# Kernel optimization log

Hardware: AMD Instinct MI355X
Metric: run time of the kernel (lower is better)

The kernel has to match this reference:

```python
import jax, jax.numpy as jnp
import numpy as np

WEIGHT = 0.1
TEMPERATURE = 0.07
EPS_NORM = 1e-12   # F.normalize eps
EPS_DEN = 1e-6     # denominator eps in pos_mask.sum()


def setup_inputs() -> dict:
    key = jax.random.key(0)
    k1, k2 = jax.random.split(key)
    features = jax.random.normal(k1, (4, 1000, 2048), dtype=jnp.float32)
    target = jax.random.randint(k2, (4, 1000), 0, 16, dtype=jnp.int64)
    return {"features": features, "target": target}


def _per_sample_loss(f, t):
    # f: [N, C], t: [N]
    N = f.shape[0]
    # F.normalize(dim=1)
    norm = jnp.maximum(jnp.linalg.norm(f, axis=1, keepdims=True), EPS_NORM)
    f = f / norm
    # [N, N] cosine similarities scaled by temperature
    sim = jnp.matmul(f, f.T) / TEMPERATURE
    eye = jnp.eye(N, dtype=f.dtype)
    pos = (t[:, None] == t[None, :]).astype(f.dtype) * (1.0 - eye)
    neg = 1.0 - pos - eye
    pos_sim = sim * pos
    # -log(exp(pos_sim) / (exp(pos_sim) + sum_j exp(sim)*neg))  summed over ALL entries
    denom = jnp.exp(pos_sim) + jnp.sum(jnp.exp(sim) * neg, axis=1, keepdims=True)
    loss_mat = jnp.log(denom) - pos_sim
    pos_sum = pos.sum()
    return loss_mat.sum() / (pos_sum + EPS_DEN), pos_sum


def reference(features, target):
    # features: [B, N, C] (already 3-D: no subsampling / interpolation paths fire)
    losses, pos_sums = jax.vmap(_per_sample_loss)(features, target)
    valid = pos_sums > 0
    num_pairs = valid.sum().astype(features.dtype)
    total = jnp.where(valid, losses, 0.0).sum()
    return jnp.where(num_pairs > 0, WEIGHT * total / num_pairs,
                     jnp.asarray(WEIGHT * 0.1, dtype=features.dtype))
```

## Files before the change

kernel.cpp:

```cpp
#include <hip/hip_runtime.h>
#include <math.h>

#define BB 4
#define NN 1000
#define NP 1024
#define CC 2048
#define TINV (1.0f / 0.07f)
#define BK 64

#define FNORM_BYTES ((size_t)BB * NP * CC * 2)
#define SIMB_BYTES  ((size_t)2 * BB * NP * NP * 2)
#define RL_BYTES    ((size_t)BB * NP * 4)

typedef __bf16 bf16x8 __attribute__((ext_vector_type(8)));
typedef float  f32x4  __attribute__((ext_vector_type(4)));
typedef float  f32x16 __attribute__((ext_vector_type(16)));

__device__ __forceinline__ void load_lds16(const void* g, void* l) {
    __builtin_amdgcn_global_load_lds(
        (const __attribute__((address_space(1))) unsigned int*)g,
        (__attribute__((address_space(3))) unsigned int*)l, 16, 0, 0);
}

__device__ __forceinline__ float blk_sum(float v, volatile float* lds) {
    int lane = threadIdx.x & 63;
    int wid  = threadIdx.x >> 6;
#pragma unroll
    for (int off = 32; off; off >>= 1) v += __shfl_down(v, off);
    __syncthreads();
    if (lane == 0) lds[wid] = v;
    __syncthreads();
    return lds[0] + lds[1] + lds[2] + lds[3];
}

__device__ __forceinline__ float wave_sum(float v) {
#pragma unroll
    for (int off = 32; off; off >>= 1) v += __shfl_down(v, off);
    return __shfl(v, 0);
}

__global__ __launch_bounds__(256) void norm_bf16_kernel(const float* __restrict__ f,
                                                        __bf16* __restrict__ out) {
    __shared__ float lds[4];
    __shared__ float scale_s;
    const int blk = blockIdx.x;
    const int b = blk >> 10, r = blk & (NP - 1);
    __bf16* dst = out + ((size_t)b * NP + r) * CC;
    const int tid = threadIdx.x;

    if (r >= NN) {
        ((uint4*)dst)[tid] = make_uint4(0u, 0u, 0u, 0u);
        return;
    }
    const float* src = f + ((size_t)b * NN + r) * CC;

    float ss = 0.f;
#pragma unroll
    for (int h = 0; h < 2; ++h) {
        float4 v = ((const float4*)src)[tid + h * 256];
        ss += v.x * v.x + v.y * v.y + v.z * v.z + v.w * v.w;
    }
    float tot = blk_sum(ss, lds);
    if (tid == 0) scale_s = 1.0f / fmaxf(sqrtf(tot), 1e-12f);
    __syncthreads();
    const float sc = scale_s;

    float4 v0 = ((const float4*)src)[tid * 2];
    float4 v1 = ((const float4*)src)[tid * 2 + 1];
    bf16x8 o;
    o[0] = (__bf16)(v0.x * sc); o[1] = (__bf16)(v0.y * sc);
    o[2] = (__bf16)(v0.z * sc); o[3] = (__bf16)(v0.w * sc);
    o[4] = (__bf16)(v1.x * sc); o[5] = (__bf16)(v1.y * sc);
    o[6] = (__bf16)(v1.z * sc); o[7] = (__bf16)(v1.w * sc);
    *(bf16x8*)(dst + tid * 8) = o;
}

__global__ __launch_bounds__(256) void simgemm_mfma(const __bf16* __restrict__ fn,
                                                    __bf16* __restrict__ simb) {
    __shared__ __bf16 As0[128 * BK], As1[128 * BK];
    __shared__ __bf16 Bs0[128 * BK], Bs1[128 * BK];

    const int bz = blockIdx.z;
    const int b  = bz >> 1;
    const int kbeg = (bz & 1) * (CC / 2);
    const int tI = blockIdx.y * 128;
    const int tJ = blockIdx.x * 128;
    const __bf16* base = fn + (size_t)b * NP * CC;
    __bf16* S = simb + (size_t)bz * NP * NP;

    const int tid  = threadIdx.x;
    const int wid  = tid >> 6;
    const int lane = tid & 63;
    const int wm   = wid >> 1;
    const int wn   = wid & 1;
    const int ln32 = lane & 31;
    const int kh   = lane >> 5;
    const int sw   = ln32 & 7;

    const int srow   = tid >> 3;
    const int schunk = (tid & 7) ^ (srow & 7);
    const __bf16* gA = base + (size_t)(tI + srow) * CC + kbeg + schunk * 8;
    const __bf16* gB = base + (size_t)(tJ + srow) * CC + kbeg + schunk * 8;
    const int wvoff = wid * 8 * BK;

    f32x16 acc[2][2] = {};

#define STAGE(k0, A, B)                                                      \
    {                                                                        \
        _Pragma("unroll")                                                    \
        for (int r = 0; r < 4; ++r)                                          \
            load_lds16(gA + (k0) + (size_t)r * 32 * CC, (A) + r * 32 * BK + wvoff); \
        _Pragma("unroll")                                                    \
        for (int r = 0; r < 4; ++r)                                          \
            load_lds16(gB + (k0) + (size_t)r * 32 * CC, (B) + r * 32 * BK + wvoff); \
    }

#define COMPUTE(A, B)                                                        \
    {                                                                        \
        _Pragma("unroll")                                                    \
        for (int kc = 0; kc < 4; ++kc) {                                     \
            const int co = ((kc * 2 + kh) ^ sw) * 8;                         \
            bf16x8 a0 = *(const bf16x8*)&(A)[(wm * 64      + ln32) * BK + co]; \
            bf16x8 a1 = *(const bf16x8*)&(A)[(wm * 64 + 32 + ln32) * BK + co]; \
            bf16x8 b0 = *(const bf16x8*)&(B)[(wn * 64      + ln32) * BK + co]; \
            bf16x8 b1 = *(const bf16x8*)&(B)[(wn * 64 + 32 + ln32) * BK + co]; \
            acc[0][0] = __builtin_amdgcn_mfma_f32_32x32x16_bf16(a0, b0, acc[0][0], 0, 0, 0); \
            acc[0][1] = __builtin_amdgcn_mfma_f32_32x32x16_bf16(a0, b1, acc[0][1], 0, 0, 0); \
            acc[1][0] = __builtin_amdgcn_mfma_f32_32x32x16_bf16(a1, b0, acc[1][0], 0, 0, 0); \
            acc[1][1] = __builtin_amdgcn_mfma_f32_32x32x16_bf16(a1, b1, acc[1][1], 0, 0, 0); \
        }                                                                    \
    }

    STAGE(0, As0, Bs0);
#pragma unroll 1
    for (int k0 = 0; k0 < CC / 2; k0 += 2 * BK) {
        __syncthreads();
        if (k0 + BK < CC / 2) STAGE(k0 + BK, As1, Bs1);
        COMPUTE(As0, Bs0);
        __syncthreads();
        if (k0 + 2 * BK < CC / 2) STAGE(k0 + 2 * BK, As0, Bs0);
        COMPUTE(As1, Bs1);
    }
#undef STAGE
#undef COMPUTE

#pragma unroll
    for (int at = 0; at < 2; ++at) {
#pragma unroll
        for (int bt = 0; bt < 2; ++bt) {
            const int col = tJ + wn * 64 + bt * 32 + ln32;
#pragma unroll
            for (int r = 0; r < 16; ++r) {
                const int row = tI + wm * 64 + at * 32 + (r & 3) + 8 * (r >> 2) + 4 * kh;
                S[(size_t)row * NP + col] = (__bf16)(acc[at][bt][r] * TINV);
            }
        }
    }
}

__global__ __launch_bounds__(256) void rowloss_kernel(const __bf16* __restrict__ simb,
                                                      const int* __restrict__ tgt,
                                                      float* __restrict__ rloss,
                                                      float* __restrict__ rpos) {
    __shared__ __align__(16) int ts[NN];
    __shared__ float rowv[4][NP];
    const int b = blockIdx.y;
    const int wid = threadIdx.x >> 6, lane = threadIdx.x & 63;
    const int* t = tgt + (size_t)b * NN;
    for (int j = threadIdx.x; j < NN; j += 256) ts[j] = t[j];
    __syncthreads();

    const int i = blockIdx.x * 4 + wid;
    const __bf16* r0 = simb + (size_t)(2 * b) * NP * NP + (size_t)i * NP;
    const __bf16* r1 = r0 + (size_t)NP * NP;
    const int ti = ts[i];

    float sneg = 0.f, pcnt = 0.f;
    for (int g = lane; g < NN / 8; g += 64) {
        bf16x8 va = ((const bf16x8*)r0)[g];
        bf16x8 vb = ((const bf16x8*)r1)[g];
        float v[8];
#pragma unroll
        for (int k = 0; k < 8; ++k) v[k] = (float)va[k] + (float)vb[k];
        *(f32x4*)&rowv[wid][g * 8]     = *(f32x4*)&v[0];
        *(f32x4*)&rowv[wid][g * 8 + 4] = *(f32x4*)&v[4];
        const int jb = g * 8;
#pragma unroll
        for (int k = 0; k < 8; ++k) {
            const int j = jb + k;
            if (j != i) {
                if (ts[j] == ti) pcnt += 1.f;
                else             sneg += __expf(v[k]);
            }
        }
    }
    const float Sv = wave_sum(sneg);
    const float p  = wave_sum(pcnt);

    float term = 0.f;
    for (int g = lane; g < NN / 8; g += 64) {
        const int jb = g * 8;
        float v[8];
        *(f32x4*)&v[0] = *(const f32x4*)&rowv[wid][jb];
        *(f32x4*)&v[4] = *(const f32x4*)&rowv[wid][jb + 4];
#pragma unroll
        for (int k = 0; k < 8; ++k) {
            const int j = jb + k;
            if (j != i && ts[j] == ti)
                term += __logf(__expf(v[k]) + Sv) - v[k];
        }
    }
    const float tt = wave_sum(term);
    if (lane == 0) {
        rloss[b * NP + i] = tt + ((float)NN - p) * __logf(1.f + Sv);
        rpos [b * NP + i] = p;
    }
}

__global__ __launch_bounds__(256) void final_kernel(const float* __restrict__ rloss,
                                                    const float* __restrict__ rpos,
                                                    float* __restrict__ out) {
    __shared__ float lds[4];
    float total = 0.f, np = 0.f;
    for (int b = 0; b < BB; ++b) {
        float l = 0.f, p = 0.f;
        for (int i = threadIdx.x; i < NN; i += 256) {
            l += rloss[b * NP + i];
            p += rpos [b * NP + i];
        }
        float ls = blk_sum(l, lds);
        float ps = blk_sum(p, lds);
        if (ps > 0.f) { total += ls / (ps + 1e-6f); np += 1.f; }
    }
    if (threadIdx.x == 0)
        out[0] = (np > 0.f) ? 0.1f * total / np : 0.1f * 0.1f;
}

extern "C" void kernel_launch(void* const* d_in, const int* in_sizes, int n_in,
                              void* d_out, int out_size, void* d_ws, size_t ws_size,
                              hipStream_t stream) {
    const float* feat = (const float*)d_in[0];
    const int*   tgt  = (const int*)d_in[1];
    char* ws = (char*)d_ws;
    __bf16* fnorm = (__bf16*)ws;                  ws += FNORM_BYTES;
    __bf16* simb  = (__bf16*)ws;                  ws += SIMB_BYTES;
    float*  rloss = (float*)ws;                   ws += RL_BYTES;
    float*  rpos  = (float*)ws;

    norm_bf16_kernel<<<dim3(BB * NP), 256, 0, stream>>>(feat, fnorm);
    simgemm_mfma<<<dim3(NP / 128, NP / 128, 2 * BB), 256, 0, stream>>>(fnorm, simb);
    rowloss_kernel<<<dim3(NN / 4, BB), 256, 0, stream>>>(simb, tgt, rloss, rpos);
    final_kernel<<<1, 256, 0, stream>>>(rloss, rpos, (float*)d_out);
}
```

Baseline: 116.1 us.

## Split GEMM K dimension four ways with smaller K tile and higher occupancy

Raises the split-K factor for the similarity GEMM from 2 to 4, which doubles the grid to 1024 blocks. It halves the K tile to 32 with a matching LDS swizzle and staging layout, and adds a launch-bounds occupancy hint of 4 blocks per CU. The goal is to fill the 256 CUs better than 512 blocks did. In exchange, the bf16 partial-sum buffer doubles, and the rowloss kernel must read and add four partial matrices, which increases memory traffic and rounding error.

```diff
diff --git a/kernel.cpp b/kernel.cpp
--- a/kernel.cpp
+++ b/kernel.cpp
@@ -6,10 +6,10 @@
 #define NP 1024
 #define CC 2048
 #define TINV (1.0f / 0.07f)
-#define BK 64
+#define BK 32
 
 #define FNORM_BYTES ((size_t)BB * NP * CC * 2)
-#define SIMB_BYTES  ((size_t)2 * BB * NP * NP * 2)
+#define SIMB_BYTES  ((size_t)4 * BB * NP * NP * 2)
 #define RL_BYTES    ((size_t)BB * NP * 4)
 
 typedef __bf16 bf16x8 __attribute__((ext_vector_type(8)));
@@ -75,14 +75,14 @@
     *(bf16x8*)(dst + tid * 8) = o;
 }
 
-__global__ __launch_bounds__(256) void simgemm_mfma(const __bf16* __restrict__ fn,
-                                                    __bf16* __restrict__ simb) {
+__global__ __launch_bounds__(256, 4) void simgemm_mfma(const __bf16* __restrict__ fn,
+                                                       __bf16* __restrict__ simb) {
     __shared__ __bf16 As0[128 * BK], As1[128 * BK];
     __shared__ __bf16 Bs0[128 * BK], Bs1[128 * BK];
 
     const int bz = blockIdx.z;
-    const int b  = bz >> 1;
-    const int kbeg = (bz & 1) * (CC / 2);
+    const int b  = bz >> 2;
+    const int kbeg = (bz & 3) * (CC / 4);
     const int tI = blockIdx.y * 128;
     const int tJ = blockIdx.x * 128;
     const __bf16* base = fn + (size_t)b * NP * CC;
@@ -95,50 +95,48 @@
     const int wn   = wid & 1;
     const int ln32 = lane & 31;
     const int kh   = lane >> 5;
-    const int sw   = ln32 & 7;
-
-    const int srow   = tid >> 3;
-    const int schunk = (tid & 7) ^ (srow & 7);
+    const int sw   = (ln32 >> 1) & 3;
+
+    const int srow   = wid * 16 + (lane >> 2);
+    const int schunk = (lane & 3) ^ ((srow >> 1) & 3);
     const __bf16* gA = base + (size_t)(tI + srow) * CC + kbeg + schunk * 8;
     const __bf16* gB = base + (size_t)(tJ + srow) * CC + kbeg + schunk * 8;
-    const int wvoff = wid * 8 * BK;
+    const int wvoff = wid * 512;
 
     f32x16 acc[2][2] = {};
 
-#define STAGE(k0, A, B)                                                      \
-    {                                                                        \
-        _Pragma("unroll")                                                    \
-        for (int r = 0; r < 4; ++r)                                          \
-            load_lds16(gA + (k0) + (size_t)r * 32 * CC, (A) + r * 32 * BK + wvoff); \
-        _Pragma("unroll")                                                    \
-        for (int r = 0; r < 4; ++r)                                          \
-            load_lds16(gB + (k0) + (size_t)r * 32 * CC, (B) + r * 32 * BK + wvoff); \
-    }
-
-#define COMPUTE(A, B)                                                        \
-    {                                                                        \
-        _Pragma("unroll")                                                    \
-        for (int kc = 0; kc < 4; ++kc) {                                     \
-            const int co = ((kc * 2 + kh) ^ sw) * 8;                         \
-            bf16x8 a0 = *(const bf16x8*)&(A)[(wm * 64      + ln32) * BK + co]; \
-            bf16x8 a1 = *(const bf16x8*)&(A)[(wm * 64 + 32 + ln32) * BK + co]; \
-            bf16x8 b0 = *(const bf16x8*)&(B)[(wn * 64      + ln32) * BK + co]; \
-            bf16x8 b1 = *(const bf16x8*)&(B)[(wn * 64 + 32 + ln32) * BK + co]; \
+#define STAGE(k0, A, B)                                            \
+    {                                                              \
+        load_lds16(gA + (k0),                   (A) + wvoff);      \
+        load_lds16(gA + (k0) + (size_t)64 * CC, (A) + 2048 + wvoff); \
+        load_lds16(gB + (k0),                   (B) + wvoff);      \
+        load_lds16(gB + (k0) + (size_t)64 * CC, (B) + 2048 + wvoff); \
+    }
+
+#define COMPUTE(A, B)                                                         \
+    {                                                                         \
+        _Pragma("unroll")                                                     \
+        for (int kc = 0; kc < 2; ++kc) {                                      \
+            const int co = ((kc * 2 + kh) ^ sw) * 8;                          \
+            bf16x8 a0 = *(const bf16x8*)&(A)[(wm * 64      + ln32) * BK + co];\
+            bf16x8 a1 = *(const bf16x8*)&(A)[(wm * 64 + 32 + ln32) * BK + co];\
+            bf16x8 b0 = *(const bf16x8*)&(B)[(wn * 64      + ln32) * BK + co];\
+            bf16x8 b1 = *(const bf16x8*)&(B)[(wn * 64 + 32 + ln32) * BK + co];\
             acc[0][0] = __builtin_amdgcn_mfma_f32_32x32x16_bf16(a0, b0, acc[0][0], 0, 0, 0); \
             acc[0][1] = __builtin_amdgcn_mfma_f32_32x32x16_bf16(a0, b1, acc[0][1], 0, 0, 0); \
             acc[1][0] = __builtin_amdgcn_mfma_f32_32x32x16_bf16(a1, b0, acc[1][0], 0, 0, 0); \
             acc[1][1] = __builtin_amdgcn_mfma_f32_32x32x16_bf16(a1, b1, acc[1][1], 0, 0, 0); \
-        }                                                                    \
+        }                                                                     \
     }
 
     STAGE(0, As0, Bs0);
 #pragma unroll 1
-    for (int k0 = 0; k0 < CC / 2; k0 += 2 * BK) {
+    for (int k0 = 0; k0 < CC / 4; k0 += 2 * BK) {
         __syncthreads();
-        if (k0 + BK < CC / 2) STAGE(k0 + BK, As1, Bs1);
+        if (k0 + BK < CC / 4) STAGE(k0 + BK, As1, Bs1);
         COMPUTE(As0, Bs0);
         __syncthreads();
-        if (k0 + 2 * BK < CC / 2) STAGE(k0 + 2 * BK, As0, Bs0);
+        if (k0 + 2 * BK < CC / 4) STAGE(k0 + 2 * BK, As0, Bs0);
         COMPUTE(As1, Bs1);
     }
 #undef STAGE
@@ -171,17 +169,22 @@
     __syncthreads();
 
     const int i = blockIdx.x * 4 + wid;
-    const __bf16* r0 = simb + (size_t)(2 * b) * NP * NP + (size_t)i * NP;
+    const __bf16* r0 = simb + (size_t)(4 * b) * NP * NP + (size_t)i * NP;
     const __bf16* r1 = r0 + (size_t)NP * NP;
+    const __bf16* r2 = r1 + (size_t)NP * NP;
+    const __bf16* r3 = r2 + (size_t)NP * NP;
     const int ti = ts[i];
 
     float sneg = 0.f, pcnt = 0.f;
     for (int g = lane; g < NN / 8; g += 64) {
         bf16x8 va = ((const bf16x8*)r0)[g];
         bf16x8 vb = ((const bf16x8*)r1)[g];
+        bf16x8 vc = ((const bf16x8*)r2)[g];
+        bf16x8 vd = ((const bf16x8*)r3)[g];
         float v[8];
 #pragma unroll
-        for (int k = 0; k < 8; ++k) v[k] = (float)va[k] + (float)vb[k];
+        for (int k = 0; k < 8; ++k)
+            v[k] = ((float)va[k] + (float)vb[k]) + ((float)vc[k] + (float)vd[k]);
         *(f32x4*)&rowv[wid][g * 8]     = *(f32x4*)&v[0];
         *(f32x4*)&rowv[wid][g * 8 + 4] = *(f32x4*)&v[4];
         const int jb = g * 8;
@@ -248,7 +251,7 @@
     float*  rpos  = (float*)ws;
 
     norm_bf16_kernel<<<dim3(BB * NP), 256, 0, stream>>>(feat, fnorm);
-    simgemm_mfma<<<dim3(NP / 128, NP / 128, 2 * BB), 256, 0, stream>>>(fnorm, simb);
+    simgemm_mfma<<<dim3(NP / 128, NP / 128, 4 * BB), 256, 0, stream>>>(fnorm, simb);
     rowloss_kernel<<<dim3(NN / 4, BB), 256, 0, stream>>>(simb, tgt, rloss, rpos);
     final_kernel<<<1, 256, 0, stream>>>(rloss, rpos, (float*)d_out);
 }
```

Result: slower. 123.4 us (+6.3%).

## Exploit Gram symmetry: compute upper-triangle tiles and mirror via LDS transpose

Applied to the files above, without the earlier changes.

The similarity GEMM now computes only the 36 upper-triangular 128x128 tiles per batch and writes each off-diagonal tile a second time, transposed through LDS, to fill the lower triangle. This roughly halves the MFMA work. To keep the grid large enough, the K dimension is split three ways (768/640/640) instead of two, and the row-loss kernel sums three partial planes. The cost is extra partial-sum traffic and memory, plus a transpose epilogue.

```diff
diff --git a/kernel.cpp b/kernel.cpp
--- a/kernel.cpp
+++ b/kernel.cpp
@@ -7,12 +7,15 @@
 #define CC 2048
 #define TINV (1.0f / 0.07f)
 #define BK 64
+#define SK 3
+#define TS 136
 
 #define FNORM_BYTES ((size_t)BB * NP * CC * 2)
-#define SIMB_BYTES  ((size_t)2 * BB * NP * NP * 2)
+#define SIMB_BYTES  ((size_t)SK * BB * NP * NP * 2)
 #define RL_BYTES    ((size_t)BB * NP * 4)
 
 typedef __bf16 bf16x8 __attribute__((ext_vector_type(8)));
+typedef __bf16 bf16x4 __attribute__((ext_vector_type(4)));
 typedef float  f32x4  __attribute__((ext_vector_type(4)));
 typedef float  f32x16 __attribute__((ext_vector_type(16)));
 
@@ -77,16 +80,18 @@
 
 __global__ __launch_bounds__(256) void simgemm_mfma(const __bf16* __restrict__ fn,
                                                     __bf16* __restrict__ simb) {
-    __shared__ __bf16 As0[128 * BK], As1[128 * BK];
-    __shared__ __bf16 Bs0[128 * BK], Bs1[128 * BK];
-
-    const int bz = blockIdx.z;
-    const int b  = bz >> 1;
-    const int kbeg = (bz & 1) * (CC / 2);
-    const int tI = blockIdx.y * 128;
-    const int tJ = blockIdx.x * 128;
+    __shared__ __align__(16) __bf16 smem[4][128 * BK];
+
+    int u = blockIdx.x, ti = 0, rem = 8;
+    while (u >= rem) { u -= rem; ++ti; --rem; }
+    const int tj = ti + u;
+    const int kq = blockIdx.y;
+    const int b  = blockIdx.z;
+    const int klen = kq ? 640 : 768;
+    const int kbeg = kq ? 768 + (kq - 1) * 640 : 0;
+    const int tI = ti * 128, tJ = tj * 128;
     const __bf16* base = fn + (size_t)b * NP * CC;
-    __bf16* S = simb + (size_t)bz * NP * NP;
+    __bf16* S = simb + (size_t)(b * SK + kq) * NP * NP;
 
     const int tid  = threadIdx.x;
     const int wid  = tid >> 6;
@@ -101,7 +106,7 @@
     const int schunk = (tid & 7) ^ (srow & 7);
     const __bf16* gA = base + (size_t)(tI + srow) * CC + kbeg + schunk * 8;
     const __bf16* gB = base + (size_t)(tJ + srow) * CC + kbeg + schunk * 8;
-    const int wvoff = wid * 8 * BK;
+    const int wvoff = wid * 512;
 
     f32x16 acc[2][2] = {};
 
@@ -131,15 +136,15 @@
         }                                                                    \
     }
 
-    STAGE(0, As0, Bs0);
+    STAGE(0, smem[0], smem[2]);
 #pragma unroll 1
-    for (int k0 = 0; k0 < CC / 2; k0 += 2 * BK) {
-        __syncthreads();
-        if (k0 + BK < CC / 2) STAGE(k0 + BK, As1, Bs1);
-        COMPUTE(As0, Bs0);
-        __syncthreads();
-        if (k0 + 2 * BK < CC / 2) STAGE(k0 + 2 * BK, As0, Bs0);
-        COMPUTE(As1, Bs1);
+    for (int k0 = 0; k0 < klen; k0 += 2 * BK) {
+        __syncthreads();
+        if (k0 + BK < klen) STAGE(k0 + BK, smem[1], smem[3]);
+        COMPUTE(smem[0], smem[2]);
+        __syncthreads();
+        if (k0 + 2 * BK < klen) STAGE(k0 + 2 * BK, smem[0], smem[2]);
+        COMPUTE(smem[1], smem[3]);
     }
 #undef STAGE
 #undef COMPUTE
@@ -155,6 +160,35 @@
                 S[(size_t)row * NP + col] = (__bf16)(acc[at][bt][r] * TINV);
             }
         }
+    }
+
+    if (ti != tj) {
+        __bf16* tsc = &smem[0][0];
+        __syncthreads();
+#pragma unroll
+        for (int at = 0; at < 2; ++at) {
+#pragma unroll
+            for (int bt = 0; bt < 2; ++bt) {
+                const int cl = wn * 64 + bt * 32 + ln32;
+#pragma unroll
+                for (int g = 0; g < 4; ++g) {
+                    const int rb = wm * 64 + at * 32 + g * 8 + 4 * kh;
+                    bf16x4 v;
+                    v[0] = (__bf16)(acc[at][bt][g * 4 + 0] * TINV);
+                    v[1] = (__bf16)(acc[at][bt][g * 4 + 1] * TINV);
+                    v[2] = (__bf16)(acc[at][bt][g * 4 + 2] * TINV);
+                    v[3] = (__bf16)(acc[at][bt][g * 4 + 3] * TINV);
+                    *(bf16x4*)&tsc[cl * TS + rb] = v;
+                }
+            }
+        }
+        __syncthreads();
+        const int jloc  = tid >> 1;
+        const int ihalf = (tid & 1) * 64;
+        const uint4* srcT = (const uint4*)&tsc[jloc * TS + ihalf];
+        uint4* dstT = (uint4*)(S + (size_t)(tJ + jloc) * NP + tI + ihalf);
+#pragma unroll
+        for (int q = 0; q < 8; ++q) dstT[q] = srcT[q];
     }
 }
 
@@ -171,17 +205,20 @@
     __syncthreads();
 
     const int i = blockIdx.x * 4 + wid;
-    const __bf16* r0 = simb + (size_t)(2 * b) * NP * NP + (size_t)i * NP;
+    const __bf16* r0 = simb + (size_t)(SK * b) * NP * NP + (size_t)i * NP;
     const __bf16* r1 = r0 + (size_t)NP * NP;
+    const __bf16* r2 = r1 + (size_t)NP * NP;
     const int ti = ts[i];
 
     float sneg = 0.f, pcnt = 0.f;
     for (int g = lane; g < NN / 8; g += 64) {
         bf16x8 va = ((const bf16x8*)r0)[g];
         bf16x8 vb = ((const bf16x8*)r1)[g];
+        bf16x8 vc = ((const bf16x8*)r2)[g];
         float v[8];
 #pragma unroll
-        for (int k = 0; k < 8; ++k) v[k] = (float)va[k] + (float)vb[k];
+        for (int k = 0; k < 8; ++k)
+            v[k] = ((float)va[k] + (float)vb[k]) + (float)vc[k];
         *(f32x4*)&rowv[wid][g * 8]     = *(f32x4*)&v[0];
         *(f32x4*)&rowv[wid][g * 8 + 4] = *(f32x4*)&v[4];
         const int jb = g * 8;
@@ -248,7 +285,7 @@
     float*  rpos  = (float*)ws;
 
     norm_bf16_kernel<<<dim3(BB * NP), 256, 0, stream>>>(feat, fnorm);
-    simgemm_mfma<<<dim3(NP / 128, NP / 128, 2 * BB), 256, 0, stream>>>(fnorm, simb);
+    simgemm_mfma<<<dim3(36, SK, BB), 256, 0, stream>>>(fnorm, simb);
     rowloss_kernel<<<dim3(NN / 4, BB), 256, 0, stream>>>(simb, tgt, rloss, rpos);
     final_kernel<<<1, 256, 0, stream>>>(rloss, rpos, (float*)d_out);
 }
```

Result: no change. 117.7 us (+1.4%).
